# Performance work log

Measured on AMD Instinct MI355X. Metric: run time of the kernel, lower is better.

Reference implementation:

```python
import jax, jax.numpy as jnp
import numpy as np

N, B, D, K, H = 30000, 16, 32, 8, 8
DIST = 5.0
EPS = 1e-6


def setup_inputs() -> dict:
    key = jax.random.key(0)
    ks = jax.random.split(key, 16)
    sc = 1.0 / np.sqrt(D)
    inp = {
        'pos': jax.random.uniform(ks[0], (N, 3), jnp.float32) * 20.0,
        'node_features': jax.random.normal(ks[1], (N, D), jnp.float32),
        'batch': jnp.sort(jax.random.randint(ks[2], (N,), 0, B, dtype=jnp.int32)),
        'bessel_weights': jnp.linspace(jnp.pi, K * jnp.pi, K).astype(jnp.float32),
        'init_dummy': jax.random.normal(ks[3], (D,), jnp.float32),
        'Wq_dummy': jax.random.normal(ks[4], (D, D), jnp.float32) * sc,
        'Wq_graph': jax.random.normal(ks[5], (D, D), jnp.float32) * sc,
        'Wdot': jax.random.normal(ks[6], (D, D), jnp.float32) * sc,
        'W1_kd': jax.random.normal(ks[7], (K, H), jnp.float32) / np.sqrt(K),
        'W2_kd': jax.random.normal(ks[8], (H, D * D), jnp.float32) / np.sqrt(H),
        'W1_vd': jax.random.normal(ks[9], (K, H), jnp.float32) / np.sqrt(K),
        'W2_vd': jax.random.normal(ks[10], (H, D * D), jnp.float32) / np.sqrt(H),
        'W1_kg': jax.random.normal(ks[11], (K, H), jnp.float32) / np.sqrt(K),
        'W2_kg': jax.random.normal(ks[12], (H, D * D), jnp.float32) / np.sqrt(H),
        'W1_vg': jax.random.normal(ks[13], (K, H), jnp.float32) / np.sqrt(K),
        'W2_vg': jax.random.normal(ks[14], (H, D * D), jnp.float32) / np.sqrt(H),
    }
    return inp


def reference(pos, node_features, batch, bessel_weights, init_dummy,
              Wq_dummy, Wq_graph, Wdot,
              W1_kd, W2_kd, W1_vd, W2_vd, W1_kg, W2_kg, W1_vg, W2_vg):
    scale = 1.0 / np.sqrt(D)

    # --- dummy edge features: per-batch z extents + bessel basis ---
    z = pos[:, 2]                                            # [N]
    z_min = jax.ops.segment_min(z, batch, num_segments=B)    # [B]
    z_max = jax.ops.segment_max(z, batch, num_segments=B)    # [B]
    bot_len = z - z_min[batch] + DIST                        # [N]
    top_len = z_max[batch] + DIST - z                        # [N]

    def bessel(x):  # [N] -> [N,K]
        return jnp.sin(bessel_weights * x[:, None]) / (x[:, None] + EPS)

    edge = jnp.stack([bessel(bot_len), bessel(top_len)], axis=1)  # [N,2,K]

    # --- init dummy node features [B, 2, D] ---
    dummy = jnp.broadcast_to(init_dummy, (B, 2, D))

    def gen_w(W1, W2):  # conditional weight generator (silu MLP)
        return (jax.nn.silu(edge @ W1) @ W2).reshape(N, 2, D, D)

    # --- dummy nodes attend over graph nodes (segment softmax) ---
    wk = gen_w(W1_kd, W2_kd)                                 # [N,2,D,D]
    wv = gen_w(W1_vd, W2_vd)
    q = (dummy @ Wq_dummy)[batch]                            # [N,2,D]
    k = jnp.einsum('nd,nsde->nse', node_features, wk)        # [N,2,D]
    v = jnp.einsum('nd,nsde->nse', node_features, wv)
    s = jnp.einsum('nsq,qk,nsk->ns', q, Wdot, k) * scale     # [N,2]
    m = jax.ops.segment_max(s, batch, num_segments=B)
    e = jnp.exp(s - m[batch])
    zsum = jax.ops.segment_sum(e, batch, num_segments=B)
    attn = e / zsum[batch]                                   # [N,2]
    dummy_new = dummy + jax.ops.segment_sum(attn[..., None] * v, batch, num_segments=B)

    # --- graph nodes attend over (2) dummy nodes ---
    wkg = gen_w(W1_kg, W2_kg)
    wvg = gen_w(W1_vg, W2_vg)
    d_per = dummy_new[batch]                                 # [N,2,D]
    kg = jnp.einsum('nsd,nsde->nse', d_per, wkg)
    vg = jnp.einsum('nsd,nsde->nse', d_per, wvg)
    qg = node_features @ Wq_graph                            # [N,D]
    sg = jnp.einsum('nq,qk,nsk->ns', qg, Wdot, kg) * scale   # [N,2]
    ag = jax.nn.softmax(sg, axis=1)
    x_new = node_features + jnp.einsum('ns,nsd->nd', ag, vg)  # [N,D]
    return x_new
```

## Files before the change

kernel.cpp:

```cpp
#include <hip/hip_runtime.h>
#include <math.h>

#define NN 30000
#define DIST_C 5.0f
#define EPS_C 1e-6f
#define SCALE_C 0.17677669529663687f

#define WS_ZSUM 0
#define WS_T    32
#define WS_CTR  8224
#define WS_ZERO_BYTES ((8224 + 16) * 4)

__device__ __forceinline__ float silu(float x) { return x / (1.0f + expf(-x)); }

__device__ __forceinline__ void bessel_edges(float bw0, float x0, float x1, float edge[2][8]) {
    float xs[2]; xs[0] = x0; xs[1] = x1;
#pragma unroll
    for (int s = 0; s < 2; ++s) {
        float x = xs[s];
        float inv = 1.0f / (x + EPS_C);
        float th = bw0 * x;
        float c2 = 2.0f * cosf(th);
        float skm1 = 0.0f;
        float sk = sinf(th);
#pragma unroll
        for (int k = 0; k < 8; ++k) {
            edge[s][k] = sk * inv;
            float nx = c2 * sk - skm1;
            skm1 = sk; sk = nx;
        }
    }
}

__global__ __launch_bounds__(256, 2) void k_mega(
    const float* __restrict__ pos, const int* __restrict__ batch,
    const float* __restrict__ nf, const float* __restrict__ bw,
    const float* __restrict__ W1_kd, const float* __restrict__ W1_vd,
    const float* __restrict__ W1_kg, const float* __restrict__ W1_vg,
    const float* __restrict__ init_dummy, const float* __restrict__ Wq_dummy,
    const float* __restrict__ Wdot, const float* __restrict__ W2_kd,
    const float* __restrict__ W2_vd, const float* __restrict__ W2_kg,
    const float* __restrict__ W2_vg, const float* __restrict__ Wq_graph,
    float* __restrict__ ws, float* __restrict__ out, int bpb)
{
    __shared__ int bnd[17];
    __shared__ float Wdl[1024];
    __shared__ float qvec[32], qWl[32];
    __shared__ __align__(16) float Pk[256];
    __shared__ __align__(16) float Wc[1024];
    __shared__ float W1kd[64], W1vd[64], W1kg[64], W1vg[64];
    __shared__ __align__(16) float Fl[32 * 36];
    __shared__ float Lw[32 * 17];
    __shared__ float zred[8];
    __shared__ float zfin[2];
    __shared__ float Tl[512], part[512], dn[64];
    __shared__ __align__(16) float AKGl[512], AVGl[512];

    int t = threadIdx.x;
    int b = blockIdx.x & 15;
    int m = blockIdx.x >> 4;
    int li = t >> 3, g = t & 7;
    int lanebase = (t & 63) & 56;
    float bw0 = bw[0];

    if (t < 17) {
        int lo = 0, hi = NN;
        while (lo < hi) { int mid = (lo + hi) >> 1; if (batch[mid] < t) lo = mid + 1; else hi = mid; }
        bnd[t] = lo;
    }
    for (int i = t; i < 1024; i += 256) Wdl[i] = Wdot[i];
    if (t < 64) { W1kd[t] = W1_kd[t]; W1vd[t] = W1_vd[t]; W1kg[t] = W1_kg[t]; W1vg[t] = W1_vg[t]; }
    if (t < 32) {
        float acc = 0.f;
        for (int d = 0; d < 32; ++d) acc += init_dummy[d] * Wq_dummy[d * 32 + t];
        qvec[t] = acc;
    }
    __syncthreads();
    int s0 = bnd[b], s1 = bnd[b + 1];

    {
        float zmn = 3.4e38f, zmx = -3.4e38f;
        for (int i = s0 + t; i < s1; i += 256) {
            float zz = pos[3 * i + 2];
            zmn = fminf(zmn, zz); zmx = fmaxf(zmx, zz);
        }
#pragma unroll
        for (int off = 1; off < 64; off <<= 1) {
            zmn = fminf(zmn, __shfl_xor(zmn, off, 64));
            zmx = fmaxf(zmx, __shfl_xor(zmx, off, 64));
        }
        if ((t & 63) == 0) { zred[(t >> 6) * 2] = zmn; zred[(t >> 6) * 2 + 1] = zmx; }
    }
    if (t < 32) {
        float acc = 0.f;
        for (int e = 0; e < 32; ++e) acc += qvec[e] * Wdl[e * 32 + t];
        qWl[t] = acc;
    }
    __syncthreads();
    if (t == 0) {
        zfin[0] = fminf(fminf(zred[0], zred[2]), fminf(zred[4], zred[6]));
        zfin[1] = fmaxf(fmaxf(zred[1], zred[3]), fmaxf(zred[5], zred[7]));
    }
    {
        int h = t >> 5, d = t & 31;
        float acc = 0.f;
        for (int e = 0; e < 32; ++e) acc += W2_kd[h * 1024 + d * 32 + e] * qWl[e];
        Pk[t] = acc;
    }
    __syncthreads();
    float zminb = zfin[0], zmaxb = zfin[1];

    float tAcc0 = 0.f, tAcc1 = 0.f, zsA0 = 0.f, zsA1 = 0.f;
    int sh = t & 15, dp = t >> 4;
    int stride = bpb * 32;
    for (int base = s0 + m * 32; base < s1; base += stride) {
        int cnt = s1 - base; if (cnt > 32) cnt = 32;
        if (li < cnt) {
            int n = base + li;
            float4 fv4 = ((const float4*)nf)[n * 8 + g];
            ((float4*)(Fl + li * 36))[g] = fv4;
            float z = pos[3 * n + 2];
            float edge[2][8];
            bessel_edges(bw0, z - zminb + DIST_C, zmaxb + DIST_C - z, edge);
            float up[8];
            const float4* Pk4 = (const float4*)Pk;
#pragma unroll
            for (int h = 0; h < 8; ++h) {
                float4 p = Pk4[h * 8 + g];
                up[h] = fv4.x * p.x + fv4.y * p.y + fv4.z * p.z + fv4.w * p.w;
            }
            float p0 = 0.f, p1 = 0.f;
#pragma unroll
            for (int k = 0; k < 8; ++k) {
                float w = W1kd[k * 8 + g];
                p0 += edge[0][k] * w; p1 += edge[1][k] * w;
            }
            float kd0 = silu(p0), kd1 = silu(p1);
            float sp0 = 0.f, sp1 = 0.f;
#pragma unroll
            for (int h = 0; h < 8; ++h) {
                sp0 += __shfl(kd0, lanebase + h, 64) * up[h];
                sp1 += __shfl(kd1, lanebase + h, 64) * up[h];
            }
#pragma unroll
            for (int mm = 1; mm < 8; mm <<= 1) {
                sp0 += __shfl_xor(sp0, mm, 64);
                sp1 += __shfl_xor(sp1, mm, 64);
            }
            float ev0 = expf(sp0 * SCALE_C);
            float ev1 = expf(sp1 * SCALE_C);
            if (g == 0) { zsA0 += ev0; zsA1 += ev1; }
            float q0 = 0.f, q1 = 0.f;
#pragma unroll
            for (int k = 0; k < 8; ++k) {
                float w = W1vd[k * 8 + g];
                q0 += edge[0][k] * w; q1 += edge[1][k] * w;
            }
            Lw[li * 17 + g] = ev0 * silu(q0);
            Lw[li * 17 + 8 + g] = ev1 * silu(q1);
        }
        __syncthreads();
        for (int i = 0; i < cnt; ++i) {
            float w = Lw[i * 17 + sh];
            float2 x = *(const float2*)(Fl + i * 36 + 2 * dp);
            tAcc0 += w * x.x; tAcc1 += w * x.y;
        }
        __syncthreads();
    }
    {
        float* Tb = ws + WS_T + b * 512 + sh * 32 + 2 * dp;
        atomicAdd(&Tb[0], tAcc0);
        atomicAdd(&Tb[1], tAcc1);
#pragma unroll
        for (int off = 1; off < 64; off <<= 1) {
            zsA0 += __shfl_xor(zsA0, off, 64);
            zsA1 += __shfl_xor(zsA1, off, 64);
        }
        if ((t & 63) == 0) { zred[(t >> 6) * 2] = zsA0; zred[(t >> 6) * 2 + 1] = zsA1; }
    }
    __syncthreads();
    if (t == 0) {
        atomicAdd(ws + WS_ZSUM + b * 2,     zred[0] + zred[2] + zred[4] + zred[6]);
        atomicAdd(ws + WS_ZSUM + b * 2 + 1, zred[1] + zred[3] + zred[5] + zred[7]);
    }
    __syncthreads();

    unsigned* ctru = (unsigned*)(ws + WS_CTR);
    if (t == 0) { __threadfence(); atomicAdd(&ctru[b], 1u); }
    for (int i = t; i < 1024; i += 256) {
        int d = i >> 5, e = i & 31;
        float acc = 0.f;
        for (int mm = 0; mm < 32; ++mm) acc += Wq_graph[d * 32 + mm] * Wdl[mm * 32 + e];
        Wc[i] = acc;
    }
    if (t == 0) {
        int guard = 0;
        while (__hip_atomic_load(&ctru[b], __ATOMIC_ACQUIRE, __HIP_MEMORY_SCOPE_AGENT)
               < (unsigned)bpb) {
            __builtin_amdgcn_s_sleep(8);
            if (++guard > (1 << 26)) break;
        }
    }
    __syncthreads();

    Tl[t]       = __hip_atomic_load(ws + WS_T + b * 512 + t,       __ATOMIC_RELAXED, __HIP_MEMORY_SCOPE_AGENT);
    Tl[256 + t] = __hip_atomic_load(ws + WS_T + b * 512 + 256 + t, __ATOMIC_RELAXED, __HIP_MEMORY_SCOPE_AGENT);
    if (t == 0) {
        zfin[0] = __hip_atomic_load(ws + WS_ZSUM + b * 2,     __ATOMIC_RELAXED, __HIP_MEMORY_SCOPE_AGENT);
        zfin[1] = __hip_atomic_load(ws + WS_ZSUM + b * 2 + 1, __ATOMIC_RELAXED, __HIP_MEMORY_SCOPE_AGENT);
    }
    __syncthreads();
    {
        int h = t >> 5, e = t & 31;
        float a0 = 0.f, a1 = 0.f;
        for (int d = 0; d < 32; ++d) {
            float w2 = W2_vd[h * 1024 + d * 32 + e];
            a0 += Tl[h * 32 + d] * w2;
            a1 += Tl[256 + h * 32 + d] * w2;
        }
        part[t] = a0; part[256 + t] = a1;
    }
    __syncthreads();
    if (t < 64) {
        int s = t >> 5, dd = t & 31;
        float acc = 0.f;
        for (int h = 0; h < 8; ++h) acc += part[s * 256 + h * 32 + dd];
        dn[t] = init_dummy[dd] + acc / zfin[s];
    }
    __syncthreads();
    {
        int h = t >> 5, e = t & 31;
        float ak0 = 0.f, av0 = 0.f, ak1 = 0.f, av1 = 0.f;
        for (int d = 0; d < 32; ++d) {
            float w2k = W2_kg[h * 1024 + d * 32 + e];
            float w2v = W2_vg[h * 1024 + d * 32 + e];
            ak0 += dn[d] * w2k;      av0 += dn[d] * w2v;
            ak1 += dn[32 + d] * w2k; av1 += dn[32 + d] * w2v;
        }
        AKGl[t] = ak0; AKGl[256 + t] = ak1;
        AVGl[t] = av0; AVGl[256 + t] = av1;
    }
    __syncthreads();

    const float4* Ak4 = (const float4*)AKGl;
    const float4* Av4 = (const float4*)AVGl;
    const float4* Wc4 = (const float4*)Wc;
    for (int base = s0 + m * 32; base < s1; base += stride) {
        int cnt = s1 - base; if (cnt > 32) cnt = 32;
        float4 fv4 = make_float4(0.f, 0.f, 0.f, 0.f);
        float z = 0.f;
        if (li < cnt) {
            int n = base + li;
            fv4 = ((const float4*)nf)[n * 8 + g];
            ((float4*)(Fl + li * 36))[g] = fv4;
            z = pos[3 * n + 2];
        }
        __syncthreads();
        if (li < cnt) {
            float edge[2][8];
            bessel_edges(bw0, z - zminb + DIST_C, zmaxb + DIST_C - z, edge);
            float sk0, sk1, sv0, sv1;
            {
                float pk0 = 0.f, pk1 = 0.f, pv0 = 0.f, pv1 = 0.f;
#pragma unroll
                for (int k = 0; k < 8; ++k) {
                    float wk = W1kg[k * 8 + g];
                    float wv = W1vg[k * 8 + g];
                    pk0 += edge[0][k] * wk; pk1 += edge[1][k] * wk;
                    pv0 += edge[0][k] * wv; pv1 += edge[1][k] * wv;
                }
                sk0 = silu(pk0); sk1 = silu(pk1);
                sv0 = silu(pv0); sv1 = silu(pv1);
            }
            float4 q4 = make_float4(0.f, 0.f, 0.f, 0.f);
            const float* myF = Fl + li * 36;
#pragma unroll
            for (int d = 0; d < 32; ++d) {
                float fd = myF[d];
                float4 w = Wc4[d * 8 + g];
                q4.x += fd * w.x; q4.y += fd * w.y; q4.z += fd * w.z; q4.w += fd * w.w;
            }
            float p0 = 0.f, p1 = 0.f;
#pragma unroll
            for (int h = 0; h < 8; ++h) {
                float4 a0 = Ak4[h * 8 + g];
                float4 a1 = Ak4[64 + h * 8 + g];
                float d0 = q4.x * a0.x + q4.y * a0.y + q4.z * a0.z + q4.w * a0.w;
                float d1 = q4.x * a1.x + q4.y * a1.y + q4.z * a1.z + q4.w * a1.w;
                p0 += __shfl(sk0, lanebase + h, 64) * d0;
                p1 += __shfl(sk1, lanebase + h, 64) * d1;
            }
#pragma unroll
            for (int mm = 1; mm < 8; mm <<= 1) {
                p0 += __shfl_xor(p0, mm, 64);
                p1 += __shfl_xor(p1, mm, 64);
            }
            float sg0 = p0 * SCALE_C, sg1 = p1 * SCALE_C;
            float mx = fmaxf(sg0, sg1);
            float e0 = expf(sg0 - mx), e1 = expf(sg1 - mx);
            float inv = 1.0f / (e0 + e1);
            float ag0 = e0 * inv, ag1 = e1 * inv;
            float4 x4 = fv4;
#pragma unroll
            for (int h = 0; h < 8; ++h) {
                float w0 = ag0 * __shfl(sv0, lanebase + h, 64);
                float w1 = ag1 * __shfl(sv1, lanebase + h, 64);
                float4 a0 = Av4[h * 8 + g];
                float4 a1 = Av4[64 + h * 8 + g];
                x4.x += w0 * a0.x + w1 * a1.x;
                x4.y += w0 * a0.y + w1 * a1.y;
                x4.z += w0 * a0.z + w1 * a1.z;
                x4.w += w0 * a0.w + w1 * a1.w;
            }
            int n = base + li;
            ((float4*)out)[n * 8 + g] = x4;
        }
        __syncthreads();
    }
}

extern "C" void kernel_launch(void* const* d_in, const int* in_sizes, int n_in,
                              void* d_out, int out_size, void* d_ws, size_t ws_size,
                              hipStream_t stream) {
    const float* pos        = (const float*)d_in[0];
    const float* nf         = (const float*)d_in[1];
    const int*   batch      = (const int*)d_in[2];
    const float* bw         = (const float*)d_in[3];
    const float* init_dummy = (const float*)d_in[4];
    const float* Wq_dummy   = (const float*)d_in[5];
    const float* Wq_graph   = (const float*)d_in[6];
    const float* Wdot       = (const float*)d_in[7];
    const float* W1_kd      = (const float*)d_in[8];
    const float* W2_kd      = (const float*)d_in[9];
    const float* W1_vd      = (const float*)d_in[10];
    const float* W2_vd      = (const float*)d_in[11];
    const float* W1_kg      = (const float*)d_in[12];
    const float* W2_kg      = (const float*)d_in[13];
    const float* W1_vg      = (const float*)d_in[14];
    const float* W2_vg      = (const float*)d_in[15];
    float* ws  = (float*)d_ws;
    float* out = (float*)d_out;

    static int bpb_cached = -1;
    if (bpb_cached < 0) {
        int maxb = 0;
        hipError_t e = hipOccupancyMaxActiveBlocksPerMultiprocessor(
            &maxb, reinterpret_cast<const void*>(k_mega), 256, 0);
        bpb_cached = (e == hipSuccess && maxb >= 2) ? 32 : 16;
    }

    hipMemsetAsync(ws, 0, WS_ZERO_BYTES, stream);
    hipLaunchKernelGGL(k_mega, dim3(16 * bpb_cached), dim3(256), 0, stream,
                       pos, batch, nf, bw, W1_kd, W1_vd, W1_kg, W1_vg,
                       init_dummy, Wq_dummy, Wdot, W2_kd, W2_vd, W2_kg, W2_vg, Wq_graph,
                       ws, out, bpb_cached);
}
```

Baseline: 136.7 us.

## Raise occupancy, double grid, prefetch first tile and cache it across phases

Raises launch bounds to 4 blocks per CU and launches 64 blocks per batch when occupancy allows, spreading nodes over more blocks. The first tile's node features and z are loaded before the z-extent reduction to hide latency. When a block has only one tile, its features, Fl shared tile and bessel edges are reused in the second phase instead of being reloaded and recomputed. The two tiny 32x32 matvecs now use all 256 threads with shuffle reductions. The higher occupancy target may cause register spills, and more blocks mean more atomics and more cross-block synchronisation cost.

```diff
diff --git a/kernel.cpp b/kernel.cpp
--- a/kernel.cpp
+++ b/kernel.cpp
@@ -32,7 +32,7 @@
     }
 }
 
-__global__ __launch_bounds__(256, 2) void k_mega(
+__global__ __launch_bounds__(256, 4) void k_mega(
     const float* __restrict__ pos, const int* __restrict__ batch,
     const float* __restrict__ nf, const float* __restrict__ bw,
     const float* __restrict__ W1_kd, const float* __restrict__ W1_vd,
@@ -70,19 +70,36 @@
     }
     for (int i = t; i < 1024; i += 256) Wdl[i] = Wdot[i];
     if (t < 64) { W1kd[t] = W1_kd[t]; W1vd[t] = W1_vd[t]; W1kg[t] = W1_kg[t]; W1vg[t] = W1_vg[t]; }
-    if (t < 32) {
-        float acc = 0.f;
-        for (int d = 0; d < 32; ++d) acc += init_dummy[d] * Wq_dummy[d * 32 + t];
-        qvec[t] = acc;
+    {
+        int o = t >> 3, j = t & 7;
+        float acc = 0.f;
+#pragma unroll
+        for (int d = 0; d < 4; ++d) acc += init_dummy[j * 4 + d] * Wq_dummy[(j * 4 + d) * 32 + o];
+        acc += __shfl_xor(acc, 1, 64);
+        acc += __shfl_xor(acc, 2, 64);
+        acc += __shfl_xor(acc, 4, 64);
+        if (j == 0) qvec[o] = acc;
     }
     __syncthreads();
     int s0 = bnd[b], s1 = bnd[b + 1];
-
+    int stride = bpb * 32;
+    int base0 = s0 + m * 32;
+
+    float4 fv4 = make_float4(0.f, 0.f, 0.f, 0.f);
+    float zz = 0.f;
+    {
+        int cnt0 = s1 - base0; if (cnt0 > 32) cnt0 = 32;
+        if (li < cnt0) {
+            int n = base0 + li;
+            fv4 = ((const float4*)nf)[n * 8 + g];
+            zz = pos[3 * n + 2];
+        }
+    }
     {
         float zmn = 3.4e38f, zmx = -3.4e38f;
         for (int i = s0 + t; i < s1; i += 256) {
-            float zz = pos[3 * i + 2];
-            zmn = fminf(zmn, zz); zmx = fmaxf(zmx, zz);
+            float v = pos[3 * i + 2];
+            zmn = fminf(zmn, v); zmx = fmaxf(zmx, v);
         }
 #pragma unroll
         for (int off = 1; off < 64; off <<= 1) {
@@ -91,12 +108,18 @@
         }
         if ((t & 63) == 0) { zred[(t >> 6) * 2] = zmn; zred[(t >> 6) * 2 + 1] = zmx; }
     }
-    if (t < 32) {
-        float acc = 0.f;
-        for (int e = 0; e < 32; ++e) acc += qvec[e] * Wdl[e * 32 + t];
-        qWl[t] = acc;
-    }
-    __syncthreads();
+    {
+        int o = t >> 3, j = t & 7;
+        float acc = 0.f;
+#pragma unroll
+        for (int e = 0; e < 4; ++e) acc += qvec[j * 4 + e] * Wdl[(j * 4 + e) * 32 + o];
+        acc += __shfl_xor(acc, 1, 64);
+        acc += __shfl_xor(acc, 2, 64);
+        acc += __shfl_xor(acc, 4, 64);
+        if (j == 0) qWl[o] = acc;
+    }
+    __syncthreads();
+
     if (t == 0) {
         zfin[0] = fminf(fminf(zred[0], zred[2]), fminf(zred[4], zred[6]));
         zfin[1] = fmaxf(fmaxf(zred[1], zred[3]), fmaxf(zred[5], zred[7]));
@@ -110,24 +133,32 @@
     __syncthreads();
     float zminb = zfin[0], zmaxb = zfin[1];
 
+    float edge[2][8];
     float tAcc0 = 0.f, tAcc1 = 0.f, zsA0 = 0.f, zsA1 = 0.f;
     int sh = t & 15, dp = t >> 4;
-    int stride = bpb * 32;
-    for (int base = s0 + m * 32; base < s1; base += stride) {
+    int aIters = 0;
+    for (int base = base0; base < s1; base += stride) {
         int cnt = s1 - base; if (cnt > 32) cnt = 32;
-        if (li < cnt) {
-            int n = base + li;
-            float4 fv4 = ((const float4*)nf)[n * 8 + g];
-            ((float4*)(Fl + li * 36))[g] = fv4;
-            float z = pos[3 * n + 2];
-            float edge[2][8];
-            bessel_edges(bw0, z - zminb + DIST_C, zmaxb + DIST_C - z, edge);
+        bool valid = li < cnt;
+        float4 f4; float zv;
+        if (aIters == 0) { f4 = fv4; zv = zz; }
+        else {
+            f4 = make_float4(0.f, 0.f, 0.f, 0.f); zv = 0.f;
+            if (valid) {
+                int n = base + li;
+                f4 = ((const float4*)nf)[n * 8 + g];
+                zv = pos[3 * n + 2];
+            }
+        }
+        if (valid) {
+            ((float4*)(Fl + li * 36))[g] = f4;
+            bessel_edges(bw0, zv - zminb + DIST_C, zmaxb + DIST_C - zv, edge);
             float up[8];
             const float4* Pk4 = (const float4*)Pk;
 #pragma unroll
             for (int h = 0; h < 8; ++h) {
                 float4 p = Pk4[h * 8 + g];
-                up[h] = fv4.x * p.x + fv4.y * p.y + fv4.z * p.z + fv4.w * p.w;
+                up[h] = f4.x * p.x + f4.y * p.y + f4.z * p.z + f4.w * p.w;
             }
             float p0 = 0.f, p1 = 0.f;
 #pragma unroll
@@ -166,6 +197,7 @@
             tAcc0 += w * x.x; tAcc1 += w * x.y;
         }
         __syncthreads();
+        ++aIters;
     }
     {
         float* Tb = ws + WS_T + b * 512 + sh * 32 + 2 * dp;
@@ -245,20 +277,26 @@
     const float4* Ak4 = (const float4*)AKGl;
     const float4* Av4 = (const float4*)AVGl;
     const float4* Wc4 = (const float4*)Wc;
-    for (int base = s0 + m * 32; base < s1; base += stride) {
+    bool firstC = true;
+    for (int base = base0; base < s1; base += stride) {
         int cnt = s1 - base; if (cnt > 32) cnt = 32;
-        float4 fv4 = make_float4(0.f, 0.f, 0.f, 0.f);
-        float z = 0.f;
-        if (li < cnt) {
-            int n = base + li;
-            fv4 = ((const float4*)nf)[n * 8 + g];
-            ((float4*)(Fl + li * 36))[g] = fv4;
-            z = pos[3 * n + 2];
-        }
-        __syncthreads();
-        if (li < cnt) {
-            float edge[2][8];
-            bessel_edges(bw0, z - zminb + DIST_C, zmaxb + DIST_C - z, edge);
+        bool valid = li < cnt;
+        bool useCache = firstC && (aIters == 1);
+        float4 f4 = fv4;
+        if (!useCache) {
+            float zv = 0.f;
+            f4 = make_float4(0.f, 0.f, 0.f, 0.f);
+            if (valid) {
+                int n = base + li;
+                f4 = ((const float4*)nf)[n * 8 + g];
+                zv = pos[3 * n + 2];
+                ((float4*)(Fl + li * 36))[g] = f4;
+            }
+            __syncthreads();
+            if (valid)
+                bessel_edges(bw0, zv - zminb + DIST_C, zmaxb + DIST_C - zv, edge);
+        }
+        if (valid) {
             float sk0, sk1, sv0, sv1;
             {
                 float pk0 = 0.f, pk1 = 0.f, pv0 = 0.f, pv1 = 0.f;
@@ -300,7 +338,7 @@
             float e0 = expf(sg0 - mx), e1 = expf(sg1 - mx);
             float inv = 1.0f / (e0 + e1);
             float ag0 = e0 * inv, ag1 = e1 * inv;
-            float4 x4 = fv4;
+            float4 x4 = f4;
 #pragma unroll
             for (int h = 0; h < 8; ++h) {
                 float w0 = ag0 * __shfl(sv0, lanebase + h, 64);
@@ -315,6 +353,7 @@
             int n = base + li;
             ((float4*)out)[n * 8 + g] = x4;
         }
+        firstC = false;
         __syncthreads();
     }
 }
@@ -346,7 +385,8 @@
         int maxb = 0;
         hipError_t e = hipOccupancyMaxActiveBlocksPerMultiprocessor(
             &maxb, reinterpret_cast<const void*>(k_mega), 256, 0);
-        bpb_cached = (e == hipSuccess && maxb >= 2) ? 32 : 16;
+        if (e != hipSuccess) maxb = 2;
+        bpb_cached = (maxb >= 4) ? 64 : ((maxb >= 2) ? 32 : 16);
     }
 
     hipMemsetAsync(ws, 0, WS_ZERO_BYTES, stream);
```

Measured after the change: 152.1 us. +11.2%, slower.
